# Kernel optimization log

Measured on AMD Instinct MI355X. Metric: run time of the kernel, lower is better.

Reference implementation:

```python
import jax, jax.numpy as jnp
import numpy as np


def setup_inputs() -> dict:
    key = jax.random.key(0)
    ks = jax.random.split(key, 4)
    B, C, H, W = 4, 256, 64, 64
    Cq = C // 8
    s_in = 1.0 / np.sqrt(C)
    return {
        "x": jax.random.normal(ks[0], (B, C, H, W), dtype=jnp.float32),
        "Wq": jax.random.normal(ks[1], (Cq, C), dtype=jnp.float32) * s_in,
        "bq": jnp.zeros((Cq,), dtype=jnp.float32),
        "Wk": jax.random.normal(ks[2], (Cq, C), dtype=jnp.float32) * s_in,
        "bk": jnp.zeros((Cq,), dtype=jnp.float32),
        "Wv": jax.random.normal(ks[3], (C, C), dtype=jnp.float32) * s_in,
        "bv": jnp.zeros((C,), dtype=jnp.float32),
    }


def reference(x, Wq, bq, Wk, bk, Wv, bv):
    B, C, H, W = x.shape
    N = H * W
    xf = x.reshape(B, C, N)  # [B, C, N] tokens
    # 1x1 convs == per-token linear projections
    Q = jnp.einsum('qc,bcn->bqn', Wq, xf) + bq[None, :, None]  # [B, C/8, N]
    K = jnp.einsum('qc,bcn->bqn', Wk, xf) + bk[None, :, None]  # [B, C/8, N]
    V = jnp.einsum('vc,bcn->bvn', Wv, xf) + bv[None, :, None]  # [B, C,   N]
    # full self-attention over spatial tokens (no scaling, per original)
    scores = jnp.einsum('bdi,bdj->bij', Q, K)      # [B, N, N]
    attn = jax.nn.softmax(scores, axis=-1)
    out = jnp.einsum('bcj,bij->bci', V, attn)       # [B, C, N]
    return out.reshape(B, C, H, W) + x
```

## Files before the change

kernel.cpp:

```cpp
#include <hip/hip_runtime.h>

typedef short short8 __attribute__((ext_vector_type(8)));
typedef float f32x4 __attribute__((ext_vector_type(4)));
typedef float f32x16 __attribute__((ext_vector_type(16)));
typedef unsigned short u16;
typedef u16 u16x8 __attribute__((ext_vector_type(8)));
typedef unsigned int u32;
typedef u32 u32x4 __attribute__((ext_vector_type(4)));

#define NTOK 4096
#define CDIM 256
#define TJ 64
#define NJT 32
#define LOG2E 1.44269504088896f

__device__ __forceinline__ u16 f2bf(float f) {
    unsigned u = __float_as_uint(f);
    unsigned r = (u + 0x7fffu + ((u >> 16) & 1u)) >> 16;
    return (u16)r;
}
__device__ __forceinline__ float bf2f(u16 h) { return __uint_as_float(((unsigned)h) << 16); }
__device__ __forceinline__ u32 pk_bf16(float a, float b) {
    u32 w;
    asm("v_cvt_pk_bf16_f32 %0, %1, %2" : "=v"(w) : "v"(a), "v"(b));
    return w;
}

__global__ __launch_bounds__(256)
void wconv(const float* __restrict__ Wq, const float* __restrict__ Wk,
           const float* __restrict__ Wv, u16* __restrict__ whi, u16* __restrict__ wlo) {
    const int row = blockIdx.x;
    const int col = threadIdx.x;
    float v;
    if (row < 32)       v = Wq[row * 256 + col] * LOG2E;
    else if (row < 64)  v = Wk[(row - 32) * 256 + col];
    else                v = Wv[(row - 64) * 256 + col];
    u16 h = f2bf(v);
    whi[row * 256 + col] = h;
    wlo[row * 256 + col] = f2bf(v - bf2f(h));
}

__global__ __launch_bounds__(256, 1)
void proj_fused(const float* __restrict__ x,
                const u16* __restrict__ whi, const u16* __restrict__ wlo,
                const float* __restrict__ bq, const float* __restrict__ bk,
                const float* __restrict__ bv,
                u16* __restrict__ qhi, u16* __restrict__ qlo,
                u16* __restrict__ khi, u16* __restrict__ klo,
                u16* __restrict__ vbf) {
    __shared__ __attribute__((aligned(16))) u16 lxh[64][260];
    __shared__ __attribute__((aligned(16))) u16 lxl[64][260];
    const int b  = blockIdx.y;
    const int n0 = blockIdx.x * 64;
    const int t  = threadIdx.x;
    const int w  = t >> 6;
    const int l  = t & 63;
    const int cl = l & 15;
    const int kg = l >> 4;

    const int sn = (t & 15) * 4;
    const int sc = t >> 4;
#pragma unroll
    for (int cc = 0; cc < 16; cc++) {
        const int c = sc + cc * 16;
        const f32x4 xv = *(const f32x4*)&x[((size_t)(b * CDIM + c)) * NTOK + n0 + sn];
#pragma unroll
        for (int i = 0; i < 4; i++) {
            u16 hh = f2bf(xv[i]);
            lxh[sn + i][c] = hh;
            lxl[sn + i][c] = f2bf(xv[i] - bf2f(hh));
        }
    }
    __syncthreads();

    f32x4 acc[5][4];
    const f32x4 fz = {0.f, 0.f, 0.f, 0.f};
#pragma unroll
    for (int i = 0; i < 5; i++)
#pragma unroll
        for (int nt = 0; nt < 4; nt++) acc[i][nt] = fz;

#pragma unroll 2
    for (int ks = 0; ks < 8; ks++) {
        const int k0 = ks * 32;
        short8 bh[4], bl[4];
#pragma unroll
        for (int nt = 0; nt < 4; nt++) {
            bh[nt] = *(const short8*)&lxh[nt * 16 + cl][k0 + kg * 8];
            bl[nt] = *(const short8*)&lxl[nt * 16 + cl][k0 + kg * 8];
        }
#pragma unroll
        for (int i = 0; i < 5; i++) {
            const int mt = w * 5 + i;
            const size_t wb = (size_t)(mt * 16 + cl) * 256 + k0 + kg * 8;
            const short8 ah = *(const short8*)&whi[wb];
            const short8 al = *(const short8*)&wlo[wb];
#pragma unroll
            for (int nt = 0; nt < 4; nt++) {
                acc[i][nt] = __builtin_amdgcn_mfma_f32_16x16x32_bf16(ah, bh[nt], acc[i][nt], 0, 0, 0);
                acc[i][nt] = __builtin_amdgcn_mfma_f32_16x16x32_bf16(ah, bl[nt], acc[i][nt], 0, 0, 0);
                acc[i][nt] = __builtin_amdgcn_mfma_f32_16x16x32_bf16(al, bh[nt], acc[i][nt], 0, 0, 0);
            }
        }
    }

#pragma unroll
    for (int i = 0; i < 5; i++) {
        const int mt = w * 5 + i;
#pragma unroll
        for (int nt = 0; nt < 4; nt++) {
            const int n = n0 + nt * 16 + cl;
#pragma unroll
            for (int r = 0; r < 4; r++) {
                const int m = kg * 4 + r;
                float v = acc[i][nt][r];
                if (mt < 2) {
                    const int ch = mt * 16 + m;
                    v += bq[ch] * LOG2E;
                    u16 hh = f2bf(v);
                    qhi[((size_t)(b * NTOK + n)) * 32 + ch] = hh;
                    qlo[((size_t)(b * NTOK + n)) * 32 + ch] = f2bf(v - bf2f(hh));
                } else if (mt < 4) {
                    const int ch = (mt - 2) * 16 + m;
                    v += bk[ch];
                    u16 hh = f2bf(v);
                    khi[((size_t)(b * NTOK + n)) * 32 + ch] = hh;
                    klo[((size_t)(b * NTOK + n)) * 32 + ch] = f2bf(v - bf2f(hh));
                } else {
                    const int c2 = (mt - 4) * 16 + m;
                    vbf[((size_t)(b * CDIM + c2)) * NTOK + n] = f2bf(v + bv[c2]);
                }
            }
        }
    }
}

__global__ __launch_bounds__(256, 2)
void attn_part(const u16* __restrict__ qhi, const u16* __restrict__ qlo,
               const u16* __restrict__ khi, const u16* __restrict__ klo,
               const u16* __restrict__ vbf,
               u16* __restrict__ pacc, float* __restrict__ pl) {
    __shared__ __attribute__((aligned(16))) u16 lkh[2][TJ][32];
    __shared__ __attribute__((aligned(16))) u16 lkl[2][TJ][32];
    __shared__ __attribute__((aligned(16))) u16 lv[2][128][72];
    float (*lt)[32][33] = reinterpret_cast<float (*)[32][33]>(&lv[0][0][0]);

    const int lin = blockIdx.x;
    const int p   = lin & 7;
    const int b   = p >> 1;
    const int h   = p & 1;
    const int js  = (lin >> 3) & 1;
    const int qb  = lin >> 4;
    const int i0  = qb * 128;
    const int jb  = js * 2048;
    const int t   = threadIdx.x;
    const int w   = t >> 6;
    const int l   = t & 63;
    const int q5  = l & 31;
    const int hi  = l >> 5;

    const int iq = i0 + w * 32 + q5;
    const size_t qbase = ((size_t)(b * NTOK + iq)) * 32;
    const short8 qh0 = *(const short8*)&qhi[qbase + hi * 8];
    const short8 qh1 = *(const short8*)&qhi[qbase + 16 + hi * 8];
    const short8 ql0 = *(const short8*)&qlo[qbase + hi * 8];
    const short8 ql1 = *(const short8*)&qlo[qbase + 16 + hi * 8];

    const int vc   = t & 127;
    const int vch0 = (t >> 7) * 4;
    const u16* vsrc = &vbf[((size_t)(b * CDIM + h * 128 + vc)) * NTOK];
    const int kj   = (t & 127) >> 1;
    const int kch2 = (t & 1) * 2;
    const u16* ksrcbase = (t < 128) ? khi : klo;
    const u16* ksrc = &ksrcbase[((size_t)(b * NTOK + kj)) * 32 + kch2 * 8];

    u16x8 vreg[4];
    u16x8 kreg0, kreg1;

    auto stage_load = [&](int tt) {
        const size_t j0 = (size_t)(jb + tt * TJ);
#pragma unroll
        for (int i = 0; i < 4; i++)
            vreg[i] = *(const u16x8*)&vsrc[j0 + (vch0 + i) * 8];
        kreg0 = *(const u16x8*)&ksrc[j0 * 32];
        kreg1 = *(const u16x8*)&ksrc[j0 * 32 + 8];
    };
    auto stage_write = [&](int buf) {
        const int s2 = (vc >> 2) & 3;
#pragma unroll
        for (int i = 0; i < 4; i++) {
            const int ci = vch0 + i;
            const int ps = (ci & 4) | ((ci ^ s2) & 3);
            *(u16x8*)&lv[buf][vc][ps * 8] = vreg[i];
        }
        const int swk = (kj >> 2) & 3;
        u16* kbase = (t < 128) ? &lkh[buf][kj][0] : &lkl[buf][kj][0];
        *(u16x8*)&kbase[((kch2)     ^ swk) * 8] = kreg0;
        *(u16x8*)&kbase[((kch2 + 1) ^ swk) * 8] = kreg1;
    };

    f32x16 acc0, acc1, acc2, acc3;
#pragma unroll
    for (int i = 0; i < 16; i++) { acc0[i] = 0.f; acc1[i] = 0.f; acc2[i] = 0.f; acc3[i] = 0.f; }
    float l_r = 0.f;

    auto qkt32 = [&](int cur, int jt) -> f32x16 {
        f32x16 s;
#pragma unroll
        for (int i = 0; i < 16; i++) s[i] = 0.f;
        const int row = jt * 32 + q5;
        const int sw  = (row >> 2) & 3;
        {
            const int ph = ((0 * 2 + hi) ^ sw) * 8;
            short8 kh = *(const short8*)&lkh[cur][row][ph];
            short8 kl = *(const short8*)&lkl[cur][row][ph];
            s = __builtin_amdgcn_mfma_f32_32x32x16_bf16(kh, qh0, s, 0, 0, 0);
            s = __builtin_amdgcn_mfma_f32_32x32x16_bf16(kl, qh0, s, 0, 0, 0);
            s = __builtin_amdgcn_mfma_f32_32x32x16_bf16(kh, ql0, s, 0, 0, 0);
        }
        {
            const int ph = ((1 * 2 + hi) ^ sw) * 8;
            short8 kh = *(const short8*)&lkh[cur][row][ph];
            short8 kl = *(const short8*)&lkl[cur][row][ph];
            s = __builtin_amdgcn_mfma_f32_32x32x16_bf16(kh, qh1, s, 0, 0, 0);
            s = __builtin_amdgcn_mfma_f32_32x32x16_bf16(kl, qh1, s, 0, 0, 0);
            s = __builtin_amdgcn_mfma_f32_32x32x16_bf16(kh, ql1, s, 0, 0, 0);
        }
        return s;
    };

    auto mkfrag = [&](u32 own0, u32 own1, u32 own2, u32 own3) -> short8 {
        const u32 sendA = hi ? own0 : own2;
        const u32 sendB = hi ? own1 : own3;
        const u32 recvA = (u32)__shfl_xor((int)sendA, 32);
        const u32 recvB = (u32)__shfl_xor((int)sendB, 32);
        u32x4 bw;
        bw[0] = hi ? recvA : own0;
        bw[1] = hi ? recvB : own1;
        bw[2] = hi ? own2 : recvA;
        bw[3] = hi ? own3 : recvB;
        return __builtin_bit_cast(short8, bw);
    };

    stage_load(0);
    stage_write(0);
    __syncthreads();

#pragma unroll 2
    for (int tt = 0; tt < NJT; ++tt) {
        const int cur = tt & 1;
        const int nxt = cur ^ 1;
        const bool pre = (tt + 1 < NJT);
        if (pre) stage_load(tt + 1);

        __builtin_amdgcn_s_setprio(1);
        f32x16 s0 = qkt32(cur, 0);
        f32x16 s1 = qkt32(cur, 1);
        __builtin_amdgcn_s_setprio(0);

#pragma unroll
        for (int i = 0; i < 16; i++) {
            s0[i] = exp2f(s0[i]);
            s1[i] = exp2f(s1[i]);
        }
        float psum = 0.f;
#pragma unroll
        for (int i = 0; i < 16; i++) psum += s0[i] + s1[i];
        l_r += psum;

        short8 pf0 = mkfrag(pk_bf16(s0[0],  s0[1]),  pk_bf16(s0[2],  s0[3]),
                            pk_bf16(s0[4],  s0[5]),  pk_bf16(s0[6],  s0[7]));
        short8 pf1 = mkfrag(pk_bf16(s0[8],  s0[9]),  pk_bf16(s0[10], s0[11]),
                            pk_bf16(s0[12], s0[13]), pk_bf16(s0[14], s0[15]));
        short8 pf2 = mkfrag(pk_bf16(s1[0],  s1[1]),  pk_bf16(s1[2],  s1[3]),
                            pk_bf16(s1[4],  s1[5]),  pk_bf16(s1[6],  s1[7]));
        short8 pf3 = mkfrag(pk_bf16(s1[8],  s1[9]),  pk_bf16(s1[10], s1[11]),
                            pk_bf16(s1[12], s1[13]), pk_bf16(s1[14], s1[15]));

        __builtin_amdgcn_s_setprio(1);
#pragma unroll
        for (int jg = 0; jg < 4; jg++) {
            const int ch = jg * 2 + hi;
            const short8 pf = (jg == 0) ? pf0 : (jg == 1) ? pf1 : (jg == 2) ? pf2 : pf3;
#define PV_CT(CT, ACC)                                                        \
            {                                                                 \
                const int row = CT * 32 + q5;                                 \
                const int sw  = (row >> 2) & 3;                               \
                const int ph  = ((ch & 4) | ((ch ^ sw) & 3)) * 8;             \
                short8 vb = *(const short8*)&lv[cur][row][ph];                \
                ACC = __builtin_amdgcn_mfma_f32_32x32x16_bf16(vb, pf, ACC, 0, 0, 0); \
            }
            PV_CT(0, acc0)
            PV_CT(1, acc1)
            PV_CT(2, acc2)
            PV_CT(3, acc3)
#undef PV_CT
        }
        __builtin_amdgcn_s_setprio(0);

        if (pre) stage_write(nxt);
        __syncthreads();
    }

    l_r += __shfl_xor(l_r, 32);
    if (h == 0 && l < 32)
        pl[((size_t)((b * 2 + js) * 32 + qb)) * 128 + w * 32 + q5] = l_r;

    const size_t tile = (size_t)(((b * 2 + h) * 2 + js) * 32 + qb);
    const int r2 = l >> 1;
    const int qc = (l & 1) * 16;
#pragma unroll
    for (int ct = 0; ct < 4; ct++) {
        const f32x16 a = (ct == 0) ? acc0 : (ct == 1) ? acc1 : (ct == 2) ? acc2 : acc3;
#pragma unroll
        for (int reg = 0; reg < 16; reg++) {
            const int crow = (reg & 3) + 8 * (reg >> 2) + 4 * hi;
            lt[w][crow][q5] = a[reg];
        }
        const int c_local = ct * 32 + r2;
        const size_t base = (tile * 128 + c_local) * 128 + w * 32 + qc;
        u32x4 pk0, pk1;
#pragma unroll
        for (int i = 0; i < 4; i++)
            pk0[i] = pk_bf16(lt[w][r2][qc + 2 * i], lt[w][r2][qc + 2 * i + 1]);
#pragma unroll
        for (int i = 0; i < 4; i++)
            pk1[i] = pk_bf16(lt[w][r2][qc + 8 + 2 * i], lt[w][r2][qc + 8 + 2 * i + 1]);
        *(u32x4*)&pacc[base]     = pk0;
        *(u32x4*)&pacc[base + 8] = pk1;
    }
}

__global__ __launch_bounds__(256)
void attn_combine(const u16* __restrict__ pacc, const float* __restrict__ pl,
                  const float* __restrict__ x, float* __restrict__ out) {
    const int g = blockIdx.x * 256 + threadIdx.x;
#pragma unroll
    for (int rep = 0; rep < 4; rep++) {
        const int f = g + rep * 131072;
        const int il8 = f & 15;
        const int qb  = (f >> 4) & 31;
        const int c   = (f >> 9) & 255;
        const int b   = f >> 17;
        const int h   = c >> 7;
        const int cl7 = c & 127;
        const size_t t0 = (size_t)(((b * 2 + h) * 2 + 0) * 32 + qb);
        const size_t t1 = t0 + 32;
        const u16x8 a0 = *(const u16x8*)&pacc[(t0 * 128 + cl7) * 128 + il8 * 8];
        const u16x8 a1 = *(const u16x8*)&pacc[(t1 * 128 + cl7) * 128 + il8 * 8];
        const size_t lb0 = ((size_t)((b * 2 + 0) * 32 + qb)) * 128 + il8 * 8;
        const size_t lb1 = ((size_t)((b * 2 + 1) * 32 + qb)) * 128 + il8 * 8;
        const f32x4 l00 = *(const f32x4*)&pl[lb0];
        const f32x4 l01 = *(const f32x4*)&pl[lb0 + 4];
        const f32x4 l10 = *(const f32x4*)&pl[lb1];
        const f32x4 l11 = *(const f32x4*)&pl[lb1 + 4];
        const size_t ox = ((size_t)(b * 256 + c)) * 4096 + qb * 128 + il8 * 8;
        const f32x4 x0 = *(const f32x4*)&x[ox];
        const f32x4 x1 = *(const f32x4*)&x[ox + 4];
        f32x4 o0, o1;
#pragma unroll
        for (int i = 0; i < 4; i++) {
            o0[i] = (bf2f(a0[i]) + bf2f(a1[i])) / (l00[i] + l10[i]) + x0[i];
            o1[i] = (bf2f(a0[4 + i]) + bf2f(a1[4 + i])) / (l01[i] + l11[i]) + x1[i];
        }
        *(f32x4*)&out[ox]     = o0;
        *(f32x4*)&out[ox + 4] = o1;
    }
}

extern "C" void kernel_launch(void* const* d_in, const int* in_sizes, int n_in,
                              void* d_out, int out_size, void* d_ws, size_t ws_size,
                              hipStream_t stream) {
    const float* x  = (const float*)d_in[0];
    const float* Wq = (const float*)d_in[1];
    const float* bq = (const float*)d_in[2];
    const float* Wk = (const float*)d_in[3];
    const float* bk = (const float*)d_in[4];
    const float* Wv = (const float*)d_in[5];
    const float* bv = (const float*)d_in[6];
    float* out = (float*)d_out;

    u16* qhi = (u16*)d_ws;
    u16* qlo = qhi + (size_t)4 * NTOK * 32;
    u16* khi = qlo + (size_t)4 * NTOK * 32;
    u16* klo = khi + (size_t)4 * NTOK * 32;
    u16* vbf = klo + (size_t)4 * NTOK * 32;
    u16* whi = vbf + (size_t)4 * CDIM * NTOK;
    u16* wlo = whi + (size_t)320 * 256;
    u16* pacc = wlo + (size_t)320 * 256;
    float* pl = (float*)(pacc + (size_t)512 * 128 * 128);

    wconv<<<dim3(320), 256, 0, stream>>>(Wq, Wk, Wv, whi, wlo);
    proj_fused<<<dim3(64, 4), 256, 0, stream>>>(x, whi, wlo, bq, bk, bv,
                                                qhi, qlo, khi, klo, vbf);
    attn_part<<<dim3(512), 256, 0, stream>>>(qhi, qlo, khi, klo, vbf, pacc, pl);
    attn_combine<<<dim3(512), 256, 0, stream>>>(pacc, pl, x, out);
}
```

Baseline: 126.7 us.

## Double query rows per wave and split keys four ways to reuse K/V tiles

Each wave now handles two 32-query sub-tiles (256 queries per block), so every K and V fragment loaded from LDS feeds twice as many MFMAs. To keep the block count at 512, the key range is split into four chunks instead of two, and the combine kernel sums four partial accumulators and row-sums. This roughly halves K/V global and LDS traffic per unit of work. In exchange it doubles accumulator registers, which may cut occupancy or cause spills, and it doubles the partial-result workspace and the combine kernel's reads.

```diff
diff --git a/kernel.cpp b/kernel.cpp
--- a/kernel.cpp
+++ b/kernel.cpp
@@ -11,7 +11,7 @@
 #define NTOK 4096
 #define CDIM 256
 #define TJ 64
-#define NJT 32
+#define NJT 16
 #define LOG2E 1.44269504088896f
 
 __device__ __forceinline__ u16 f2bf(float f) {
@@ -149,22 +149,27 @@
     const int p   = lin & 7;
     const int b   = p >> 1;
     const int h   = p & 1;
-    const int js  = (lin >> 3) & 1;
-    const int qb  = lin >> 4;
-    const int i0  = qb * 128;
-    const int jb  = js * 2048;
+    const int js  = (lin >> 3) & 3;
+    const int qp  = lin >> 5;
+    const int i0  = qp * 256;
+    const int jb  = js * 1024;
     const int t   = threadIdx.x;
     const int w   = t >> 6;
     const int l   = t & 63;
     const int q5  = l & 31;
     const int hi  = l >> 5;
 
-    const int iq = i0 + w * 32 + q5;
-    const size_t qbase = ((size_t)(b * NTOK + iq)) * 32;
-    const short8 qh0 = *(const short8*)&qhi[qbase + hi * 8];
-    const short8 qh1 = *(const short8*)&qhi[qbase + 16 + hi * 8];
-    const short8 ql0 = *(const short8*)&qlo[qbase + hi * 8];
-    const short8 ql1 = *(const short8*)&qlo[qbase + 16 + hi * 8];
+    const int iqA = i0 + w * 64 + q5;
+    const size_t qbA = ((size_t)(b * NTOK + iqA)) * 32;
+    const size_t qbB = qbA + 32 * 32;
+    const short8 qAh0 = *(const short8*)&qhi[qbA + hi * 8];
+    const short8 qAh1 = *(const short8*)&qhi[qbA + 16 + hi * 8];
+    const short8 qAl0 = *(const short8*)&qlo[qbA + hi * 8];
+    const short8 qAl1 = *(const short8*)&qlo[qbA + 16 + hi * 8];
+    const short8 qBh0 = *(const short8*)&qhi[qbB + hi * 8];
+    const short8 qBh1 = *(const short8*)&qhi[qbB + 16 + hi * 8];
+    const short8 qBl0 = *(const short8*)&qlo[qbB + hi * 8];
+    const short8 qBl1 = *(const short8*)&qlo[qbB + 16 + hi * 8];
 
     const int vc   = t & 127;
     const int vch0 = (t >> 7) * 4;
@@ -199,35 +204,14 @@
         *(u16x8*)&kbase[((kch2 + 1) ^ swk) * 8] = kreg1;
     };
 
-    f32x16 acc0, acc1, acc2, acc3;
-#pragma unroll
-    for (int i = 0; i < 16; i++) { acc0[i] = 0.f; acc1[i] = 0.f; acc2[i] = 0.f; acc3[i] = 0.f; }
-    float l_r = 0.f;
-
-    auto qkt32 = [&](int cur, int jt) -> f32x16 {
-        f32x16 s;
-#pragma unroll
-        for (int i = 0; i < 16; i++) s[i] = 0.f;
-        const int row = jt * 32 + q5;
-        const int sw  = (row >> 2) & 3;
-        {
-            const int ph = ((0 * 2 + hi) ^ sw) * 8;
-            short8 kh = *(const short8*)&lkh[cur][row][ph];
-            short8 kl = *(const short8*)&lkl[cur][row][ph];
-            s = __builtin_amdgcn_mfma_f32_32x32x16_bf16(kh, qh0, s, 0, 0, 0);
-            s = __builtin_amdgcn_mfma_f32_32x32x16_bf16(kl, qh0, s, 0, 0, 0);
-            s = __builtin_amdgcn_mfma_f32_32x32x16_bf16(kh, ql0, s, 0, 0, 0);
-        }
-        {
-            const int ph = ((1 * 2 + hi) ^ sw) * 8;
-            short8 kh = *(const short8*)&lkh[cur][row][ph];
-            short8 kl = *(const short8*)&lkl[cur][row][ph];
-            s = __builtin_amdgcn_mfma_f32_32x32x16_bf16(kh, qh1, s, 0, 0, 0);
-            s = __builtin_amdgcn_mfma_f32_32x32x16_bf16(kl, qh1, s, 0, 0, 0);
-            s = __builtin_amdgcn_mfma_f32_32x32x16_bf16(kh, ql1, s, 0, 0, 0);
-        }
-        return s;
-    };
+    f32x16 accA0, accA1, accA2, accA3;
+    f32x16 accB0, accB1, accB2, accB3;
+#pragma unroll
+    for (int i = 0; i < 16; i++) {
+        accA0[i] = 0.f; accA1[i] = 0.f; accA2[i] = 0.f; accA3[i] = 0.f;
+        accB0[i] = 0.f; accB1[i] = 0.f; accB2[i] = 0.f; accB3[i] = 0.f;
+    }
+    float l_rA = 0.f, l_rB = 0.f;
 
     auto mkfrag = [&](u32 own0, u32 own1, u32 own2, u32 own3) -> short8 {
         const u32 sendA = hi ? own0 : own2;
@@ -253,81 +237,119 @@
         const bool pre = (tt + 1 < NJT);
         if (pre) stage_load(tt + 1);
 
-        __builtin_amdgcn_s_setprio(1);
-        f32x16 s0 = qkt32(cur, 0);
-        f32x16 s1 = qkt32(cur, 1);
-        __builtin_amdgcn_s_setprio(0);
-
-#pragma unroll
-        for (int i = 0; i < 16; i++) {
-            s0[i] = exp2f(s0[i]);
-            s1[i] = exp2f(s1[i]);
-        }
-        float psum = 0.f;
-#pragma unroll
-        for (int i = 0; i < 16; i++) psum += s0[i] + s1[i];
-        l_r += psum;
-
-        short8 pf0 = mkfrag(pk_bf16(s0[0],  s0[1]),  pk_bf16(s0[2],  s0[3]),
-                            pk_bf16(s0[4],  s0[5]),  pk_bf16(s0[6],  s0[7]));
-        short8 pf1 = mkfrag(pk_bf16(s0[8],  s0[9]),  pk_bf16(s0[10], s0[11]),
-                            pk_bf16(s0[12], s0[13]), pk_bf16(s0[14], s0[15]));
-        short8 pf2 = mkfrag(pk_bf16(s1[0],  s1[1]),  pk_bf16(s1[2],  s1[3]),
-                            pk_bf16(s1[4],  s1[5]),  pk_bf16(s1[6],  s1[7]));
-        short8 pf3 = mkfrag(pk_bf16(s1[8],  s1[9]),  pk_bf16(s1[10], s1[11]),
-                            pk_bf16(s1[12], s1[13]), pk_bf16(s1[14], s1[15]));
-
-        __builtin_amdgcn_s_setprio(1);
-#pragma unroll
-        for (int jg = 0; jg < 4; jg++) {
-            const int ch = jg * 2 + hi;
-            const short8 pf = (jg == 0) ? pf0 : (jg == 1) ? pf1 : (jg == 2) ? pf2 : pf3;
-#define PV_CT(CT, ACC)                                                        \
-            {                                                                 \
-                const int row = CT * 32 + q5;                                 \
-                const int sw  = (row >> 2) & 3;                               \
-                const int ph  = ((ch & 4) | ((ch ^ sw) & 3)) * 8;             \
-                short8 vb = *(const short8*)&lv[cur][row][ph];                \
-                ACC = __builtin_amdgcn_mfma_f32_32x32x16_bf16(vb, pf, ACC, 0, 0, 0); \
-            }
-            PV_CT(0, acc0)
-            PV_CT(1, acc1)
-            PV_CT(2, acc2)
-            PV_CT(3, acc3)
+#pragma unroll
+        for (int jt = 0; jt < 2; jt++) {
+            const int row = jt * 32 + q5;
+            const int sw  = (row >> 2) & 3;
+            const int ph0 = ((hi) ^ sw) * 8;
+            const int ph1 = ((2 + hi) ^ sw) * 8;
+            const short8 kh0 = *(const short8*)&lkh[cur][row][ph0];
+            const short8 kl0 = *(const short8*)&lkl[cur][row][ph0];
+            const short8 kh1 = *(const short8*)&lkh[cur][row][ph1];
+            const short8 kl1 = *(const short8*)&lkl[cur][row][ph1];
+
+            f32x16 sA, sB;
+#pragma unroll
+            for (int i = 0; i < 16; i++) { sA[i] = 0.f; sB[i] = 0.f; }
+            __builtin_amdgcn_s_setprio(1);
+            sA = __builtin_amdgcn_mfma_f32_32x32x16_bf16(kh0, qAh0, sA, 0, 0, 0);
+            sA = __builtin_amdgcn_mfma_f32_32x32x16_bf16(kl0, qAh0, sA, 0, 0, 0);
+            sA = __builtin_amdgcn_mfma_f32_32x32x16_bf16(kh0, qAl0, sA, 0, 0, 0);
+            sA = __builtin_amdgcn_mfma_f32_32x32x16_bf16(kh1, qAh1, sA, 0, 0, 0);
+            sA = __builtin_amdgcn_mfma_f32_32x32x16_bf16(kl1, qAh1, sA, 0, 0, 0);
+            sA = __builtin_amdgcn_mfma_f32_32x32x16_bf16(kh1, qAl1, sA, 0, 0, 0);
+            sB = __builtin_amdgcn_mfma_f32_32x32x16_bf16(kh0, qBh0, sB, 0, 0, 0);
+            sB = __builtin_amdgcn_mfma_f32_32x32x16_bf16(kl0, qBh0, sB, 0, 0, 0);
+            sB = __builtin_amdgcn_mfma_f32_32x32x16_bf16(kh0, qBl0, sB, 0, 0, 0);
+            sB = __builtin_amdgcn_mfma_f32_32x32x16_bf16(kh1, qBh1, sB, 0, 0, 0);
+            sB = __builtin_amdgcn_mfma_f32_32x32x16_bf16(kl1, qBh1, sB, 0, 0, 0);
+            sB = __builtin_amdgcn_mfma_f32_32x32x16_bf16(kh1, qBl1, sB, 0, 0, 0);
+            __builtin_amdgcn_s_setprio(0);
+
+#pragma unroll
+            for (int i = 0; i < 16; i++) {
+                sA[i] = exp2f(sA[i]);
+                sB[i] = exp2f(sB[i]);
+            }
+            float psA = 0.f, psB = 0.f;
+#pragma unroll
+            for (int i = 0; i < 16; i++) { psA += sA[i]; psB += sB[i]; }
+            l_rA += psA;
+            l_rB += psB;
+
+            short8 pfA0 = mkfrag(pk_bf16(sA[0],  sA[1]),  pk_bf16(sA[2],  sA[3]),
+                                 pk_bf16(sA[4],  sA[5]),  pk_bf16(sA[6],  sA[7]));
+            short8 pfA1 = mkfrag(pk_bf16(sA[8],  sA[9]),  pk_bf16(sA[10], sA[11]),
+                                 pk_bf16(sA[12], sA[13]), pk_bf16(sA[14], sA[15]));
+            short8 pfB0 = mkfrag(pk_bf16(sB[0],  sB[1]),  pk_bf16(sB[2],  sB[3]),
+                                 pk_bf16(sB[4],  sB[5]),  pk_bf16(sB[6],  sB[7]));
+            short8 pfB1 = mkfrag(pk_bf16(sB[8],  sB[9]),  pk_bf16(sB[10], sB[11]),
+                                 pk_bf16(sB[12], sB[13]), pk_bf16(sB[14], sB[15]));
+
+            __builtin_amdgcn_s_setprio(1);
+#pragma unroll
+            for (int jgl = 0; jgl < 2; jgl++) {
+                const int ch = (jt * 2 + jgl) * 2 + hi;
+                const short8 pfA = jgl ? pfA1 : pfA0;
+                const short8 pfB = jgl ? pfB1 : pfB0;
+#define PV_CT(CT, ACCA, ACCB)                                                 \
+                {                                                             \
+                    const int vrow = CT * 32 + q5;                            \
+                    const int vsw  = (vrow >> 2) & 3;                         \
+                    const int vph  = ((ch & 4) | ((ch ^ vsw) & 3)) * 8;       \
+                    short8 vb = *(const short8*)&lv[cur][vrow][vph];          \
+                    ACCA = __builtin_amdgcn_mfma_f32_32x32x16_bf16(vb, pfA, ACCA, 0, 0, 0); \
+                    ACCB = __builtin_amdgcn_mfma_f32_32x32x16_bf16(vb, pfB, ACCB, 0, 0, 0); \
+                }
+                PV_CT(0, accA0, accB0)
+                PV_CT(1, accA1, accB1)
+                PV_CT(2, accA2, accB2)
+                PV_CT(3, accA3, accB3)
 #undef PV_CT
-        }
-        __builtin_amdgcn_s_setprio(0);
+            }
+            __builtin_amdgcn_s_setprio(0);
+        }
 
         if (pre) stage_write(nxt);
         __syncthreads();
     }
 
-    l_r += __shfl_xor(l_r, 32);
-    if (h == 0 && l < 32)
-        pl[((size_t)((b * 2 + js) * 32 + qb)) * 128 + w * 32 + q5] = l_r;
-
-    const size_t tile = (size_t)(((b * 2 + h) * 2 + js) * 32 + qb);
+    l_rA += __shfl_xor(l_rA, 32);
+    l_rB += __shfl_xor(l_rB, 32);
+    if (h == 0 && l < 32) {
+        const size_t plb = (size_t)(b * 4 + js) * NTOK + i0 + w * 64;
+        pl[plb + q5]      = l_rA;
+        pl[plb + 32 + q5] = l_rB;
+    }
+
+    const size_t tile = (size_t)(((b * 2 + h) * 4 + js) * 16 + qp);
     const int r2 = l >> 1;
     const int qc = (l & 1) * 16;
 #pragma unroll
-    for (int ct = 0; ct < 4; ct++) {
-        const f32x16 a = (ct == 0) ? acc0 : (ct == 1) ? acc1 : (ct == 2) ? acc2 : acc3;
-#pragma unroll
-        for (int reg = 0; reg < 16; reg++) {
-            const int crow = (reg & 3) + 8 * (reg >> 2) + 4 * hi;
-            lt[w][crow][q5] = a[reg];
-        }
-        const int c_local = ct * 32 + r2;
-        const size_t base = (tile * 128 + c_local) * 128 + w * 32 + qc;
-        u32x4 pk0, pk1;
-#pragma unroll
-        for (int i = 0; i < 4; i++)
-            pk0[i] = pk_bf16(lt[w][r2][qc + 2 * i], lt[w][r2][qc + 2 * i + 1]);
-#pragma unroll
-        for (int i = 0; i < 4; i++)
-            pk1[i] = pk_bf16(lt[w][r2][qc + 8 + 2 * i], lt[w][r2][qc + 8 + 2 * i + 1]);
-        *(u32x4*)&pacc[base]     = pk0;
-        *(u32x4*)&pacc[base + 8] = pk1;
+    for (int sub = 0; sub < 2; sub++) {
+#pragma unroll
+        for (int ct = 0; ct < 4; ct++) {
+            const f32x16 a =
+                (sub == 0)
+                    ? ((ct == 0) ? accA0 : (ct == 1) ? accA1 : (ct == 2) ? accA2 : accA3)
+                    : ((ct == 0) ? accB0 : (ct == 1) ? accB1 : (ct == 2) ? accB2 : accB3);
+#pragma unroll
+            for (int reg = 0; reg < 16; reg++) {
+                const int crow = (reg & 3) + 8 * (reg >> 2) + 4 * hi;
+                lt[w][crow][q5] = a[reg];
+            }
+            const int c_local = ct * 32 + r2;
+            const size_t base = (tile * 128 + c_local) * 256 + w * 64 + sub * 32 + qc;
+            u32x4 pk0, pk1;
+#pragma unroll
+            for (int i = 0; i < 4; i++)
+                pk0[i] = pk_bf16(lt[w][r2][qc + 2 * i], lt[w][r2][qc + 2 * i + 1]);
+#pragma unroll
+            for (int i = 0; i < 4; i++)
+                pk1[i] = pk_bf16(lt[w][r2][qc + 8 + 2 * i], lt[w][r2][qc + 8 + 2 * i + 1]);
+            *(u32x4*)&pacc[base]     = pk0;
+            *(u32x4*)&pacc[base + 8] = pk1;
+        }
     }
 }
 
@@ -338,30 +360,39 @@
 #pragma unroll
     for (int rep = 0; rep < 4; rep++) {
         const int f = g + rep * 131072;
-        const int il8 = f & 15;
-        const int qb  = (f >> 4) & 31;
+        const int il8 = f & 31;
+        const int qp  = (f >> 5) & 15;
         const int c   = (f >> 9) & 255;
         const int b   = f >> 17;
         const int h   = c >> 7;
         const int cl7 = c & 127;
-        const size_t t0 = (size_t)(((b * 2 + h) * 2 + 0) * 32 + qb);
-        const size_t t1 = t0 + 32;
-        const u16x8 a0 = *(const u16x8*)&pacc[(t0 * 128 + cl7) * 128 + il8 * 8];
-        const u16x8 a1 = *(const u16x8*)&pacc[(t1 * 128 + cl7) * 128 + il8 * 8];
-        const size_t lb0 = ((size_t)((b * 2 + 0) * 32 + qb)) * 128 + il8 * 8;
-        const size_t lb1 = ((size_t)((b * 2 + 1) * 32 + qb)) * 128 + il8 * 8;
-        const f32x4 l00 = *(const f32x4*)&pl[lb0];
-        const f32x4 l01 = *(const f32x4*)&pl[lb0 + 4];
-        const f32x4 l10 = *(const f32x4*)&pl[lb1];
-        const f32x4 l11 = *(const f32x4*)&pl[lb1 + 4];
-        const size_t ox = ((size_t)(b * 256 + c)) * 4096 + qb * 128 + il8 * 8;
+        f32x4 as0 = {0.f, 0.f, 0.f, 0.f};
+        f32x4 as1 = {0.f, 0.f, 0.f, 0.f};
+        f32x4 ls0 = {0.f, 0.f, 0.f, 0.f};
+        f32x4 ls1 = {0.f, 0.f, 0.f, 0.f};
+#pragma unroll
+        for (int js = 0; js < 4; js++) {
+            const size_t tile = (size_t)(((b * 2 + h) * 4 + js) * 16 + qp);
+            const u16x8 a = *(const u16x8*)&pacc[(tile * 128 + cl7) * 256 + il8 * 8];
+            const size_t lb = (size_t)(b * 4 + js) * 4096 + qp * 256 + il8 * 8;
+            const f32x4 l0 = *(const f32x4*)&pl[lb];
+            const f32x4 l1 = *(const f32x4*)&pl[lb + 4];
+#pragma unroll
+            for (int i = 0; i < 4; i++) {
+                as0[i] += bf2f(a[i]);
+                as1[i] += bf2f(a[4 + i]);
+                ls0[i] += l0[i];
+                ls1[i] += l1[i];
+            }
+        }
+        const size_t ox = ((size_t)(b * 256 + c)) * 4096 + qp * 256 + il8 * 8;
         const f32x4 x0 = *(const f32x4*)&x[ox];
         const f32x4 x1 = *(const f32x4*)&x[ox + 4];
         f32x4 o0, o1;
 #pragma unroll
         for (int i = 0; i < 4; i++) {
-            o0[i] = (bf2f(a0[i]) + bf2f(a1[i])) / (l00[i] + l10[i]) + x0[i];
-            o1[i] = (bf2f(a0[4 + i]) + bf2f(a1[4 + i])) / (l01[i] + l11[i]) + x1[i];
+            o0[i] = as0[i] / ls0[i] + x0[i];
+            o1[i] = as1[i] / ls1[i] + x1[i];
         }
         *(f32x4*)&out[ox]     = o0;
         *(f32x4*)&out[ox + 4] = o1;
@@ -388,7 +419,7 @@
     u16* whi = vbf + (size_t)4 * CDIM * NTOK;
     u16* wlo = whi + (size_t)320 * 256;
     u16* pacc = wlo + (size_t)320 * 256;
-    float* pl = (float*)(pacc + (size_t)512 * 128 * 128);
+    float* pl = (float*)(pacc + (size_t)512 * 128 * 256);
 
     wconv<<<dim3(320), 256, 0, stream>>>(Wq, Wk, Wv, whi, wlo);
     proj_fused<<<dim3(64, 4), 256, 0, stream>>>(x, whi, wlo, bq, bk, bv,
```

Measured after the change: 300.2 us. 2.37x slower.
